# Kernel tuning notes

Measured on AMD Instinct MI355X. Metric: run time of the kernel, lower is better.

The kernel has to match this reference:

```python
import jax, jax.numpy as jnp
import numpy as np

B, L, N, D = 4096, 50, 50, 128
STD = 0.1


def setup_inputs() -> dict:
    key = jax.random.key(0)
    ks = jax.random.split(key, 6)
    seq_idx = jax.random.randint(ks[0], (B, L), 0, N, dtype=jnp.int32)
    mask = jnp.ones((B, L), dtype=jnp.int32)
    node_vectors = jax.random.normal(ks[1], (B, N, D), dtype=jnp.float32)
    u = lambda k, shp: jax.random.uniform(k, shp, jnp.float32, -STD, STD)
    return {
        "sequence_of_indexes": seq_idx,
        "mask": mask,
        "node_vectors": node_vectors,
        "batch_size": B,
        "W_last": u(ks[2], (D, D)),      # dense_last_item kernel (no bias)
        "W_seq": u(ks[3], (D, D)),       # dense_sequence_items kernel
        "b_seq": jnp.zeros((D,), jnp.float32),  # dense_sequence_items bias
        "W_alpha": u(ks[4], (D, 1)),     # dense_alpha kernel (no bias)
    }


def reference(sequence_of_indexes, mask, node_vectors, batch_size,
              W_last, W_seq, b_seq, W_alpha):
    maskf = mask.astype(jnp.float32)                          # [B, L]
    seq_len = jnp.sum(maskf, axis=1).astype(jnp.int32)        # [B]
    rows = jnp.arange(batch_size)
    # last item index per session, then gather its node vector
    last_idx = sequence_of_indexes[rows, seq_len - 1]         # [B]
    v_n = node_vectors[rows, last_idx]                        # [B, D]
    # per-batch embedding lookup: node_vectors[b, seq_idx[b]]
    v_i = jnp.take_along_axis(node_vectors, sequence_of_indexes[..., None], axis=1)  # [B, L, D]
    vn_proj = (v_n @ W_last)[:, None, :]                      # [B, 1, D]
    vi_proj = v_i @ W_seq + b_seq                             # [B, L, D]
    alpha = jax.nn.sigmoid(vn_proj + vi_proj) @ W_alpha       # [B, L, 1]
    alpha = alpha * maskf[..., None]
    session_graph = jnp.sum(alpha * v_i, axis=1)              # [B, D]
    return v_n, session_graph
```

## Files before the change

### kernel.cpp

```cpp
#include <hip/hip_runtime.h>
#include <math.h>

#define BB 4096
#define LL 50
#define NN 50
#define DD 128

typedef short bf16x8 __attribute__((ext_vector_type(8)));
typedef float f32x4  __attribute__((ext_vector_type(4)));

static __device__ inline unsigned short f32_to_bf16_rne(float f) {
    unsigned int u = __float_as_uint(f);
    u += 0x7FFFu + ((u >> 16) & 1u);
    return (unsigned short)(u >> 16);
}

static __device__ inline bf16x8 pack8(float4 lo, float4 hi) {
    bf16x8 r;
    r[0] = (short)f32_to_bf16_rne(lo.x);
    r[1] = (short)f32_to_bf16_rne(lo.y);
    r[2] = (short)f32_to_bf16_rne(lo.z);
    r[3] = (short)f32_to_bf16_rne(lo.w);
    r[4] = (short)f32_to_bf16_rne(hi.x);
    r[5] = (short)f32_to_bf16_rne(hi.y);
    r[6] = (short)f32_to_bf16_rne(hi.z);
    r[7] = (short)f32_to_bf16_rne(hi.w);
    return r;
}

__global__ void prep_w(const float* __restrict__ W_seq,
                       const float* __restrict__ W_last,
                       unsigned short* __restrict__ ws)
{
    int t = blockIdx.x * blockDim.x + threadIdx.x;
    int lane = t & 63;
    int nt   = (t >> 6) & 7;
    int kk   = t >> 9;
    const float* W = (kk < 4) ? W_seq : W_last;
    int kb = (kk & 3) * 32 + (lane >> 4) * 8;
    int n  = nt * 16 + (lane & 15);
    unsigned short* dst = ws + (size_t)t * 8;
    #pragma unroll
    for (int j = 0; j < 8; ++j)
        dst[j] = f32_to_bf16_rne(W[(kb + j) * DD + n]);
}

__global__ __launch_bounds__(256, 4) void sess_attn(
    const int*   __restrict__ seq_idx,
    const int*   __restrict__ mask,
    const float* __restrict__ nodes,
    const float* __restrict__ b_seq,
    const float* __restrict__ W_alpha,
    const unsigned short* __restrict__ wfrag,
    float*       __restrict__ out)
{
    const int b    = blockIdx.x;
    const int tid  = threadIdx.x;
    const int lane = tid & 63;
    const int wave = tid >> 6;
    const int col  = lane & 15;
    const int quad = lane >> 4;

    __shared__ __align__(16) float s_f[NN * DD];
    __shared__ float s_alpha[64];
    __shared__ float s_cnt[64];
    __shared__ int   s_last;

    const float* nb = nodes + (size_t)b * (NN * DD);

    int pm = 0, pi = 0;
    if (tid < 64) {
        pm = (tid < LL) ? mask[b * LL + tid]    : 0;
        pi = (tid < LL) ? seq_idx[b * LL + tid] : 0;
    }

    #pragma unroll
    for (int i = 0; i < 6; ++i) {
        int p  = i * 256 + tid;
        int r  = p >> 5;
        int Bk = p & 31;
        const float* src = nb + r * DD + ((Bk ^ (r & 7)) << 2);
        __builtin_amdgcn_global_load_lds(
            (const __attribute__((address_space(1))) unsigned int*)src,
            (__attribute__((address_space(3))) unsigned int*)(&s_f[(i * 256 + wave * 64) * 4]),
            16, 0, 0);
    }
    if (tid < 64) {
        int p  = 1536 + tid;
        int r  = p >> 5, Bk = p & 31;
        const float* src = nb + r * DD + ((Bk ^ (r & 7)) << 2);
        __builtin_amdgcn_global_load_lds(
            (const __attribute__((address_space(1))) unsigned int*)src,
            (__attribute__((address_space(3))) unsigned int*)(&s_f[1536 * 4]),
            16, 0, 0);
    }

    const bf16x8* wsf = (const bf16x8*)wfrag;
    bf16x8 bfS[8];
    #pragma unroll
    for (int kk = 0; kk < 4; ++kk)
        #pragma unroll
        for (int j2 = 0; j2 < 2; ++j2)
            bfS[kk * 2 + j2] = wsf[(size_t)((kk * 8 + wave * 2 + j2) * 64 + lane)];

    float bb_r[2], wa_r[2];
    #pragma unroll
    for (int j2 = 0; j2 < 2; ++j2) {
        int n = (wave * 2 + j2) * 16 + col;
        bb_r[j2] = b_seq[n];
        wa_r[j2] = W_alpha[n];
    }

    if (tid < 64) {
        s_alpha[tid] = 0.f;
        s_cnt[tid]   = 0.f;
        int mm = pm;
        mm += __shfl_xor(mm, 1);  mm += __shfl_xor(mm, 2);
        mm += __shfl_xor(mm, 4);  mm += __shfl_xor(mm, 8);
        mm += __shfl_xor(mm, 16); mm += __shfl_xor(mm, 32);
        int jl = mm - 1;
        if (jl < 0) jl += LL;
        int li = __shfl(pi, jl);
        if (tid == 0) s_last = li;
        if (tid < LL && pm) atomicAdd(&s_cnt[pi], (float)pm);
    }

    __syncthreads();

    const int last = s_last;
    const int sL   = last & 7;

    if (tid < DD)
        out[(size_t)b * DD + tid] =
            s_f[last * DD + (((tid >> 2) ^ sL) << 2) + (tid & 3)];

    f32x4 acc[4][2];
    #pragma unroll
    for (int m = 0; m < 4; ++m)
        #pragma unroll
        for (int j2 = 0; j2 < 2; ++j2)
            acc[m][j2] = (f32x4){0.f, 0.f, 0.f, 0.f};
    f32x4 accV[2];
    #pragma unroll
    for (int j2 = 0; j2 < 2; ++j2)
        accV[j2] = (f32x4){bb_r[j2], bb_r[j2], bb_r[j2], bb_r[j2]};

    #pragma unroll
    for (int kk = 0; kk < 4; ++kk) {
        const int B1 = kk * 8 + quad * 2;
        bf16x8 a[4];
        #pragma unroll
        for (int m = 0; m < 4; ++m) {
            int r = m * 16 + col;
            if (r > NN - 1) r = NN - 1;
            int s = r & 7;
            float4 lo = *(const float4*)&s_f[r * DD + ((B1 ^ s) << 2)];
            float4 hi = *(const float4*)&s_f[r * DD + (((B1 + 1) ^ s) << 2)];
            a[m] = pack8(lo, hi);
        }
        float4 vlo = *(const float4*)&s_f[last * DD + ((B1 ^ sL) << 2)];
        float4 vhi = *(const float4*)&s_f[last * DD + (((B1 + 1) ^ sL) << 2)];
        bf16x8 av = pack8(vlo, vhi);
        #pragma unroll
        for (int j2 = 0; j2 < 2; ++j2) {
            bf16x8 bl = wsf[(size_t)(((kk + 4) * 8 + wave * 2 + j2) * 64 + lane)];
            acc[0][j2] = __builtin_amdgcn_mfma_f32_16x16x32_bf16(a[0], bfS[kk * 2 + j2], acc[0][j2], 0, 0, 0);
            acc[1][j2] = __builtin_amdgcn_mfma_f32_16x16x32_bf16(a[1], bfS[kk * 2 + j2], acc[1][j2], 0, 0, 0);
            acc[2][j2] = __builtin_amdgcn_mfma_f32_16x16x32_bf16(a[2], bfS[kk * 2 + j2], acc[2][j2], 0, 0, 0);
            acc[3][j2] = __builtin_amdgcn_mfma_f32_16x16x32_bf16(a[3], bfS[kk * 2 + j2], acc[3][j2], 0, 0, 0);
            accV[j2]   = __builtin_amdgcn_mfma_f32_16x16x32_bf16(av,   bl,              accV[j2],   0, 0, 0);
        }
    }

    #pragma unroll
    for (int m = 0; m < 4; ++m) {
        float pr[4] = {0.f, 0.f, 0.f, 0.f};
        #pragma unroll
        for (int j2 = 0; j2 < 2; ++j2) {
            float waj = wa_r[j2];
            #pragma unroll
            for (int r = 0; r < 4; ++r) {
                float x = acc[m][j2][r] + accV[j2][r];
                float sig = 1.f / (1.f + __expf(-x));
                pr[r] = fmaf(sig, waj, pr[r]);
            }
        }
        #pragma unroll
        for (int r = 0; r < 4; ++r) {
            float vv = pr[r];
            vv += __shfl_xor(vv, 1);
            vv += __shfl_xor(vv, 2);
            vv += __shfl_xor(vv, 4);
            vv += __shfl_xor(vv, 8);
            int row = m * 16 + quad * 4 + r;
            if (col == 0 && row < NN) atomicAdd(&s_alpha[row], vv);
        }
    }
    __syncthreads();

    if (tid < DD) {
        const int Bd = tid >> 2, od = tid & 3;
        float acc2 = 0.f;
        #pragma unroll 10
        for (int n = 0; n < NN; ++n)
            acc2 = fmaf(s_cnt[n] * s_alpha[n],
                        s_f[n * DD + ((Bd ^ (n & 7)) << 2) + od], acc2);
        out[(size_t)BB * DD + (size_t)b * DD + tid] = acc2;
    }
}

extern "C" void kernel_launch(void* const* d_in, const int* in_sizes, int n_in,
                              void* d_out, int out_size, void* d_ws, size_t ws_size,
                              hipStream_t stream) {
    const int*   seq     = (const int*)  d_in[0];
    const int*   mask    = (const int*)  d_in[1];
    const float* nodes   = (const float*)d_in[2];
    const float* W_last  = (const float*)d_in[4];
    const float* W_seq   = (const float*)d_in[5];
    const float* b_seq   = (const float*)d_in[6];
    const float* W_alpha = (const float*)d_in[7];
    float*       out     = (float*)      d_out;

    unsigned short* wsf = (unsigned short*)d_ws;

    prep_w<<<16, 256, 0, stream>>>(W_seq, W_last, wsf);
    sess_attn<<<BB, 256, 0, stream>>>(seq, mask, nodes, b_seq, W_alpha, wsf, out);
}
```

Before: 191.3 us.

## Process two sessions per block with bf16 LDS tiles converted once

Each block now handles two batch rows. Node vectors are loaded into registers, converted to bf16 once, and stored into padded LDS tiles (stride 136), replacing the per-MFMA fp32-to-bf16 packing from swizzled fp32 LDS. The last-item output is read directly from global memory, and the final weighted sum uses the bf16 copies with two accumulators. This cuts repeated conversion work and LDS footprint per session and amortises the weight-fragment loads across two sessions. In exchange it drops the async global-to-LDS loads, halves the grid, and lowers the precision of the session_graph sum.

```diff
diff --git a/kernel.cpp b/kernel.cpp
--- a/kernel.cpp
+++ b/kernel.cpp
@@ -5,6 +5,7 @@
 #define LL 50
 #define NN 50
 #define DD 128
+#define STR 136
 
 typedef short bf16x8 __attribute__((ext_vector_type(8)));
 typedef float f32x4  __attribute__((ext_vector_type(4)));
@@ -14,18 +15,8 @@
     u += 0x7FFFu + ((u >> 16) & 1u);
     return (unsigned short)(u >> 16);
 }
-
-static __device__ inline bf16x8 pack8(float4 lo, float4 hi) {
-    bf16x8 r;
-    r[0] = (short)f32_to_bf16_rne(lo.x);
-    r[1] = (short)f32_to_bf16_rne(lo.y);
-    r[2] = (short)f32_to_bf16_rne(lo.z);
-    r[3] = (short)f32_to_bf16_rne(lo.w);
-    r[4] = (short)f32_to_bf16_rne(hi.x);
-    r[5] = (short)f32_to_bf16_rne(hi.y);
-    r[6] = (short)f32_to_bf16_rne(hi.z);
-    r[7] = (short)f32_to_bf16_rne(hi.w);
-    return r;
+static __device__ inline float bf16_to_f32(unsigned short h) {
+    return __uint_as_float(((unsigned int)h) << 16);
 }
 
 __global__ void prep_w(const float* __restrict__ W_seq,
@@ -54,46 +45,35 @@
     const unsigned short* __restrict__ wfrag,
     float*       __restrict__ out)
 {
-    const int b    = blockIdx.x;
+    const int b0   = blockIdx.x * 2;
+    const int b1   = b0 + 1;
     const int tid  = threadIdx.x;
     const int lane = tid & 63;
     const int wave = tid >> 6;
     const int col  = lane & 15;
     const int quad = lane >> 4;
 
-    __shared__ __align__(16) float s_f[NN * DD];
-    __shared__ float s_alpha[64];
-    __shared__ float s_cnt[64];
-    __shared__ int   s_last;
-
-    const float* nb = nodes + (size_t)b * (NN * DD);
+    __shared__ __align__(16) unsigned short s_t0[NN * STR];
+    __shared__ __align__(16) unsigned short s_t1[NN * STR];
+    __shared__ float s_alpha0[64], s_cnt0[64];
+    __shared__ float s_alpha1[64], s_cnt1[64];
+    __shared__ int   s_last0, s_last1;
 
     int pm = 0, pi = 0;
-    if (tid < 64) {
-        pm = (tid < LL) ? mask[b * LL + tid]    : 0;
-        pi = (tid < LL) ? seq_idx[b * LL + tid] : 0;
-    }
-
-    #pragma unroll
-    for (int i = 0; i < 6; ++i) {
-        int p  = i * 256 + tid;
-        int r  = p >> 5;
-        int Bk = p & 31;
-        const float* src = nb + r * DD + ((Bk ^ (r & 7)) << 2);
-        __builtin_amdgcn_global_load_lds(
-            (const __attribute__((address_space(1))) unsigned int*)src,
-            (__attribute__((address_space(3))) unsigned int*)(&s_f[(i * 256 + wave * 64) * 4]),
-            16, 0, 0);
-    }
-    if (tid < 64) {
-        int p  = 1536 + tid;
-        int r  = p >> 5, Bk = p & 31;
-        const float* src = nb + r * DD + ((Bk ^ (r & 7)) << 2);
-        __builtin_amdgcn_global_load_lds(
-            (const __attribute__((address_space(1))) unsigned int*)src,
-            (__attribute__((address_space(3))) unsigned int*)(&s_f[1536 * 4]),
-            16, 0, 0);
-    }
+    if (tid < 128) {
+        int bb = (wave == 0) ? b0 : b1;
+        pm = (lane < LL) ? mask[bb * LL + lane]    : 0;
+        pi = (lane < LL) ? seq_idx[bb * LL + lane] : 0;
+    }
+
+    const float4* nb0 = (const float4*)(nodes + (size_t)b0 * (NN * DD));
+    const float4* nb1 = (const float4*)(nodes + (size_t)b1 * (NN * DD));
+    float4 va[6], vb[6], vat, vbt;
+    #pragma unroll
+    for (int j = 0; j < 6; ++j) va[j] = nb0[tid + j * 256];
+    #pragma unroll
+    for (int j = 0; j < 6; ++j) vb[j] = nb1[tid + j * 256];
+    if (tid < 64) { vat = nb0[1536 + tid]; vbt = nb1[1536 + tid]; }
 
     const bf16x8* wsf = (const bf16x8*)wfrag;
     bf16x8 bfS[8];
@@ -111,9 +91,34 @@
         wa_r[j2] = W_alpha[n];
     }
 
+    if (tid < 64)                 { s_alpha0[tid]  = 0.f; s_cnt0[tid]  = 0.f; }
+    else if (tid < 128)           { s_alpha1[lane] = 0.f; s_cnt1[lane] = 0.f; }
+
+    #pragma unroll
+    for (int j = 0; j < 6; ++j) {
+        int idx = tid + j * 256;
+        int r = idx >> 5, c = (idx & 31) * 4;
+        ushort4 h;
+        h.x = f32_to_bf16_rne(va[j].x); h.y = f32_to_bf16_rne(va[j].y);
+        h.z = f32_to_bf16_rne(va[j].z); h.w = f32_to_bf16_rne(va[j].w);
+        *(ushort4*)&s_t0[r * STR + c] = h;
+        h.x = f32_to_bf16_rne(vb[j].x); h.y = f32_to_bf16_rne(vb[j].y);
+        h.z = f32_to_bf16_rne(vb[j].z); h.w = f32_to_bf16_rne(vb[j].w);
+        *(ushort4*)&s_t1[r * STR + c] = h;
+    }
     if (tid < 64) {
-        s_alpha[tid] = 0.f;
-        s_cnt[tid]   = 0.f;
+        int idx = 1536 + tid;
+        int r = idx >> 5, c = (idx & 31) * 4;
+        ushort4 h;
+        h.x = f32_to_bf16_rne(vat.x); h.y = f32_to_bf16_rne(vat.y);
+        h.z = f32_to_bf16_rne(vat.z); h.w = f32_to_bf16_rne(vat.w);
+        *(ushort4*)&s_t0[r * STR + c] = h;
+        h.x = f32_to_bf16_rne(vbt.x); h.y = f32_to_bf16_rne(vbt.y);
+        h.z = f32_to_bf16_rne(vbt.z); h.w = f32_to_bf16_rne(vbt.w);
+        *(ushort4*)&s_t1[r * STR + c] = h;
+    }
+
+    if (tid < 128) {
         int mm = pm;
         mm += __shfl_xor(mm, 1);  mm += __shfl_xor(mm, 2);
         mm += __shfl_xor(mm, 4);  mm += __shfl_xor(mm, 8);
@@ -121,91 +126,152 @@
         int jl = mm - 1;
         if (jl < 0) jl += LL;
         int li = __shfl(pi, jl);
-        if (tid == 0) s_last = li;
-        if (tid < LL && pm) atomicAdd(&s_cnt[pi], (float)pm);
+        if (lane == 0) { if (wave == 0) s_last0 = li; else s_last1 = li; }
+        if (lane < LL && pm)
+            atomicAdd((wave == 0) ? &s_cnt0[pi] : &s_cnt1[pi], (float)pm);
     }
 
     __syncthreads();
 
-    const int last = s_last;
-    const int sL   = last & 7;
-
-    if (tid < DD)
-        out[(size_t)b * DD + tid] =
-            s_f[last * DD + (((tid >> 2) ^ sL) << 2) + (tid & 3)];
-
-    f32x4 acc[4][2];
-    #pragma unroll
-    for (int m = 0; m < 4; ++m)
+    const int last0 = s_last0, last1 = s_last1;
+
+    if (tid < 128)
+        out[(size_t)b0 * DD + tid] =
+            nodes[(size_t)b0 * (NN * DD) + last0 * DD + tid];
+    else
+        out[(size_t)b1 * DD + (tid - 128)] =
+            nodes[(size_t)b1 * (NN * DD) + last1 * DD + (tid - 128)];
+
+    const int r0 = col, r1 = 16 + col, r2 = 32 + col;
+    const int r3 = (48 + col > NN - 1) ? (NN - 1) : (48 + col);
+
+    {
+        f32x4 acc[4][2], accV[2];
+        #pragma unroll
+        for (int m = 0; m < 4; ++m)
+            #pragma unroll
+            for (int j2 = 0; j2 < 2; ++j2)
+                acc[m][j2] = (f32x4){0.f, 0.f, 0.f, 0.f};
         #pragma unroll
         for (int j2 = 0; j2 < 2; ++j2)
-            acc[m][j2] = (f32x4){0.f, 0.f, 0.f, 0.f};
-    f32x4 accV[2];
-    #pragma unroll
-    for (int j2 = 0; j2 < 2; ++j2)
-        accV[j2] = (f32x4){bb_r[j2], bb_r[j2], bb_r[j2], bb_r[j2]};
-
-    #pragma unroll
-    for (int kk = 0; kk < 4; ++kk) {
-        const int B1 = kk * 8 + quad * 2;
-        bf16x8 a[4];
+            accV[j2] = (f32x4){bb_r[j2], bb_r[j2], bb_r[j2], bb_r[j2]};
+
+        #pragma unroll
+        for (int kk = 0; kk < 4; ++kk) {
+            const int co = kk * 32 + quad * 8;
+            bf16x8 a0 = *(const bf16x8*)&s_t0[r0 * STR + co];
+            bf16x8 a1 = *(const bf16x8*)&s_t0[r1 * STR + co];
+            bf16x8 a2 = *(const bf16x8*)&s_t0[r2 * STR + co];
+            bf16x8 a3 = *(const bf16x8*)&s_t0[r3 * STR + co];
+            bf16x8 av = *(const bf16x8*)&s_t0[last0 * STR + co];
+            #pragma unroll
+            for (int j2 = 0; j2 < 2; ++j2) {
+                bf16x8 bl = wsf[(size_t)(((kk + 4) * 8 + wave * 2 + j2) * 64 + lane)];
+                acc[0][j2] = __builtin_amdgcn_mfma_f32_16x16x32_bf16(a0, bfS[kk * 2 + j2], acc[0][j2], 0, 0, 0);
+                acc[1][j2] = __builtin_amdgcn_mfma_f32_16x16x32_bf16(a1, bfS[kk * 2 + j2], acc[1][j2], 0, 0, 0);
+                acc[2][j2] = __builtin_amdgcn_mfma_f32_16x16x32_bf16(a2, bfS[kk * 2 + j2], acc[2][j2], 0, 0, 0);
+                acc[3][j2] = __builtin_amdgcn_mfma_f32_16x16x32_bf16(a3, bfS[kk * 2 + j2], acc[3][j2], 0, 0, 0);
+                accV[j2]   = __builtin_amdgcn_mfma_f32_16x16x32_bf16(av, bl,               accV[j2],   0, 0, 0);
+            }
+        }
+
         #pragma unroll
         for (int m = 0; m < 4; ++m) {
-            int r = m * 16 + col;
-            if (r > NN - 1) r = NN - 1;
-            int s = r & 7;
-            float4 lo = *(const float4*)&s_f[r * DD + ((B1 ^ s) << 2)];
-            float4 hi = *(const float4*)&s_f[r * DD + (((B1 + 1) ^ s) << 2)];
-            a[m] = pack8(lo, hi);
-        }
-        float4 vlo = *(const float4*)&s_f[last * DD + ((B1 ^ sL) << 2)];
-        float4 vhi = *(const float4*)&s_f[last * DD + (((B1 + 1) ^ sL) << 2)];
-        bf16x8 av = pack8(vlo, vhi);
-        #pragma unroll
-        for (int j2 = 0; j2 < 2; ++j2) {
-            bf16x8 bl = wsf[(size_t)(((kk + 4) * 8 + wave * 2 + j2) * 64 + lane)];
-            acc[0][j2] = __builtin_amdgcn_mfma_f32_16x16x32_bf16(a[0], bfS[kk * 2 + j2], acc[0][j2], 0, 0, 0);
-            acc[1][j2] = __builtin_amdgcn_mfma_f32_16x16x32_bf16(a[1], bfS[kk * 2 + j2], acc[1][j2], 0, 0, 0);
-            acc[2][j2] = __builtin_amdgcn_mfma_f32_16x16x32_bf16(a[2], bfS[kk * 2 + j2], acc[2][j2], 0, 0, 0);
-            acc[3][j2] = __builtin_amdgcn_mfma_f32_16x16x32_bf16(a[3], bfS[kk * 2 + j2], acc[3][j2], 0, 0, 0);
-            accV[j2]   = __builtin_amdgcn_mfma_f32_16x16x32_bf16(av,   bl,              accV[j2],   0, 0, 0);
-        }
-    }
-
-    #pragma unroll
-    for (int m = 0; m < 4; ++m) {
-        float pr[4] = {0.f, 0.f, 0.f, 0.f};
-        #pragma unroll
-        for (int j2 = 0; j2 < 2; ++j2) {
-            float waj = wa_r[j2];
+            float pr[4] = {0.f, 0.f, 0.f, 0.f};
+            #pragma unroll
+            for (int j2 = 0; j2 < 2; ++j2) {
+                float waj = wa_r[j2];
+                #pragma unroll
+                for (int r = 0; r < 4; ++r) {
+                    float x = acc[m][j2][r] + accV[j2][r];
+                    pr[r] = fmaf(1.f / (1.f + __expf(-x)), waj, pr[r]);
+                }
+            }
             #pragma unroll
             for (int r = 0; r < 4; ++r) {
-                float x = acc[m][j2][r] + accV[j2][r];
-                float sig = 1.f / (1.f + __expf(-x));
-                pr[r] = fmaf(sig, waj, pr[r]);
-            }
-        }
-        #pragma unroll
-        for (int r = 0; r < 4; ++r) {
-            float vv = pr[r];
-            vv += __shfl_xor(vv, 1);
-            vv += __shfl_xor(vv, 2);
-            vv += __shfl_xor(vv, 4);
-            vv += __shfl_xor(vv, 8);
-            int row = m * 16 + quad * 4 + r;
-            if (col == 0 && row < NN) atomicAdd(&s_alpha[row], vv);
-        }
-    }
+                float vv = pr[r];
+                vv += __shfl_xor(vv, 1);
+                vv += __shfl_xor(vv, 2);
+                vv += __shfl_xor(vv, 4);
+                vv += __shfl_xor(vv, 8);
+                int row = m * 16 + quad * 4 + r;
+                if (col == 0 && row < NN) atomicAdd(&s_alpha0[row], vv);
+            }
+        }
+    }
+
+    {
+        f32x4 acc[4][2], accV[2];
+        #pragma unroll
+        for (int m = 0; m < 4; ++m)
+            #pragma unroll
+            for (int j2 = 0; j2 < 2; ++j2)
+                acc[m][j2] = (f32x4){0.f, 0.f, 0.f, 0.f};
+        #pragma unroll
+        for (int j2 = 0; j2 < 2; ++j2)
+            accV[j2] = (f32x4){bb_r[j2], bb_r[j2], bb_r[j2], bb_r[j2]};
+
+        #pragma unroll
+        for (int kk = 0; kk < 4; ++kk) {
+            const int co = kk * 32 + quad * 8;
+            bf16x8 a0 = *(const bf16x8*)&s_t1[r0 * STR + co];
+            bf16x8 a1 = *(const bf16x8*)&s_t1[r1 * STR + co];
+            bf16x8 a2 = *(const bf16x8*)&s_t1[r2 * STR + co];
+            bf16x8 a3 = *(const bf16x8*)&s_t1[r3 * STR + co];
+            bf16x8 av = *(const bf16x8*)&s_t1[last1 * STR + co];
+            #pragma unroll
+            for (int j2 = 0; j2 < 2; ++j2) {
+                bf16x8 bl = wsf[(size_t)(((kk + 4) * 8 + wave * 2 + j2) * 64 + lane)];
+                acc[0][j2] = __builtin_amdgcn_mfma_f32_16x16x32_bf16(a0, bfS[kk * 2 + j2], acc[0][j2], 0, 0, 0);
+                acc[1][j2] = __builtin_amdgcn_mfma_f32_16x16x32_bf16(a1, bfS[kk * 2 + j2], acc[1][j2], 0, 0, 0);
+                acc[2][j2] = __builtin_amdgcn_mfma_f32_16x16x32_bf16(a2, bfS[kk * 2 + j2], acc[2][j2], 0, 0, 0);
+                acc[3][j2] = __builtin_amdgcn_mfma_f32_16x16x32_bf16(a3, bfS[kk * 2 + j2], acc[3][j2], 0, 0, 0);
+                accV[j2]   = __builtin_amdgcn_mfma_f32_16x16x32_bf16(av, bl,               accV[j2],   0, 0, 0);
+            }
+        }
+
+        #pragma unroll
+        for (int m = 0; m < 4; ++m) {
+            float pr[4] = {0.f, 0.f, 0.f, 0.f};
+            #pragma unroll
+            for (int j2 = 0; j2 < 2; ++j2) {
+                float waj = wa_r[j2];
+                #pragma unroll
+                for (int r = 0; r < 4; ++r) {
+                    float x = acc[m][j2][r] + accV[j2][r];
+                    pr[r] = fmaf(1.f / (1.f + __expf(-x)), waj, pr[r]);
+                }
+            }
+            #pragma unroll
+            for (int r = 0; r < 4; ++r) {
+                float vv = pr[r];
+                vv += __shfl_xor(vv, 1);
+                vv += __shfl_xor(vv, 2);
+                vv += __shfl_xor(vv, 4);
+                vv += __shfl_xor(vv, 8);
+                int row = m * 16 + quad * 4 + r;
+                if (col == 0 && row < NN) atomicAdd(&s_alpha1[row], vv);
+            }
+        }
+    }
+
     __syncthreads();
 
-    if (tid < DD) {
-        const int Bd = tid >> 2, od = tid & 3;
-        float acc2 = 0.f;
-        #pragma unroll 10
-        for (int n = 0; n < NN; ++n)
-            acc2 = fmaf(s_cnt[n] * s_alpha[n],
-                        s_f[n * DD + ((Bd ^ (n & 7)) << 2) + od], acc2);
-        out[(size_t)BB * DD + (size_t)b * DD + tid] = acc2;
+    {
+        const int d  = tid & 127;
+        const unsigned short* st = (tid < 128) ? s_t0 : s_t1;
+        const float* sc = (tid < 128) ? s_cnt0 : s_cnt1;
+        const float* sa = (tid < 128) ? s_alpha0 : s_alpha1;
+        const int ob = (tid < 128) ? b0 : b1;
+        float accA = 0.f, accB = 0.f;
+        #pragma unroll 5
+        for (int n = 0; n < NN; n += 2) {
+            float wA = sc[n]     * sa[n];
+            float wB = sc[n + 1] * sa[n + 1];
+            accA = fmaf(wA, bf16_to_f32(st[n * STR + d]), accA);
+            accB = fmaf(wB, bf16_to_f32(st[(n + 1) * STR + d]), accB);
+        }
+        out[(size_t)BB * DD + (size_t)ob * DD + d] = accA + accB;
     }
 }
 
@@ -224,5 +290,5 @@
     unsigned short* wsf = (unsigned short*)d_ws;
 
     prep_w<<<16, 256, 0, stream>>>(W_seq, W_last, wsf);
-    sess_attn<<<BB, 256, 0, stream>>>(seq, mask, nodes, b_seq, W_alpha, wsf, out);
-}
+    sess_attn<<<BB / 2, 256, 0, stream>>>(seq, mask, nodes, b_seq, W_alpha, wsf, out);
+}
```

Result: faster. 186.6 us (-2.5%).
